# Kernel tuning notes

Hardware: AMD Instinct MI355X
Metric: run time of the kernel (lower is better)

Reference implementation:

```python
import jax, jax.numpy as jnp
import numpy as np

INPUT_DIM = 20000
UNITS = 4096
NNZ = 2_000_000
BATCH = 2048


def setup_inputs() -> dict:
    key = jax.random.key(0)
    k1, k2, k3, k4 = jax.random.split(key, 4)
    x = jax.random.normal(k1, (BATCH, INPUT_DIM), dtype=jnp.float32)
    kernel_vector = jax.random.normal(k2, (NNZ,), dtype=jnp.float32) * 0.05
    bias = jnp.zeros((UNITS,), dtype=jnp.float32)
    rows = jax.random.randint(k3, (NNZ,), 0, INPUT_DIM, dtype=jnp.int32)
    cols = jax.random.randint(k4, (NNZ,), 0, UNITS, dtype=jnp.int32)
    nonzero_ind = jnp.stack([rows, cols], axis=1)  # (NNZ, 2)
    return {"x": x, "kernel_vector": kernel_vector, "bias": bias, "nonzero_ind": nonzero_ind}


def reference(x, kernel_vector, bias, nonzero_ind):
    # scatter_nd: build dense (input_dim, units) kernel from COO representation.
    # Duplicate indices accumulate (tf.scatter_nd semantics) -> use .add.
    trans = jnp.zeros((INPUT_DIM, UNITS), dtype=kernel_vector.dtype)
    trans = trans.at[nonzero_ind[:, 0], nonzero_ind[:, 1]].add(kernel_vector)
    out = x @ trans + bias  # (batch, units)
    return jnp.tanh(out)
```

## Files before the change

kernel.cpp:

```cpp
#include <hip/hip_runtime.h>
#include <cstdint>
#include <cstddef>

#define M_DIM 2048
#define N_DIM 4096
#define K_DIM 20000
#define KP    20480
#define KZ    10240
#define NITER 80
#define WBT_BYTES  167772160UL
#define XB_OFFSET  167772160UL
#define CP_OFFSET  251658240UL

typedef __attribute__((ext_vector_type(8))) short short8;
typedef __attribute__((ext_vector_type(4))) float float4v;
typedef __attribute__((ext_vector_type(8))) unsigned short ushort8;

__device__ __forceinline__ unsigned short f2bf_rne(float f) {
    union { float f; unsigned int u; } v; v.f = f;
    unsigned int u = v.u;
    u += 0x7FFFu + ((u >> 16) & 1u);
    return (unsigned short)(u >> 16);
}

__device__ __forceinline__ float bf2f(unsigned short h) {
    union { unsigned int u; float f; } v;
    v.u = ((unsigned int)h) << 16;
    return v.f;
}

__device__ __forceinline__ void gload_lds16(const void* g, void* l) {
    __builtin_amdgcn_global_load_lds(
        (const __attribute__((address_space(1))) void*)g,
        (__attribute__((address_space(3))) void*)l, 16, 0, 0);
}

__global__ void scatter_bf16_kernel(const float* __restrict__ kv,
                                    const int* __restrict__ ind,
                                    unsigned int* __restrict__ W, int nnz) {
    int t = blockIdx.x * blockDim.x + threadIdx.x;
    if (t >= nnz) return;
    int r = ind[2 * t];
    int c = ind[2 * t + 1];
    float v = kv[t];
    size_t elem = (size_t)c * KP + r;
    unsigned int* word = &W[elem >> 1];
    const bool hi = (elem & 1) != 0;
    unsigned int old = __atomic_load_n(word, __ATOMIC_RELAXED);
    unsigned int assumed;
    do {
        assumed = old;
        unsigned short h = hi ? (unsigned short)(assumed >> 16)
                              : (unsigned short)(assumed & 0xFFFFu);
        unsigned short nh = f2bf_rne(bf2f(h) + v);
        unsigned int nw = hi ? ((assumed & 0x0000FFFFu) | ((unsigned int)nh << 16))
                             : ((assumed & 0xFFFF0000u) | (unsigned int)nh);
        old = atomicCAS(word, assumed, nw);
    } while (old != assumed);
}

__global__ void convert_kernel(const float* __restrict__ src,
                               unsigned short* __restrict__ dst) {
    size_t t = (size_t)blockIdx.x * 256 + threadIdx.x;
    int row = (int)(t / 2560);
    int c8  = (int)(t % 2560);
    ushort8 o;
    if (c8 < 2500) {
        const float4* sv = (const float4*)(src + (size_t)row * K_DIM + (size_t)c8 * 8);
        float4 a = sv[0];
        float4 b = sv[1];
        o[0] = f2bf_rne(a.x); o[1] = f2bf_rne(a.y);
        o[2] = f2bf_rne(a.z); o[3] = f2bf_rne(a.w);
        o[4] = f2bf_rne(b.x); o[5] = f2bf_rne(b.y);
        o[6] = f2bf_rne(b.z); o[7] = f2bf_rne(b.w);
    } else {
        o = (ushort8)0;
    }
    *(ushort8*)(dst + (size_t)row * KP + (size_t)c8 * 8) = o;
}

__global__ __launch_bounds__(512, 2) void gemm256_kernel(
    const unsigned short* __restrict__ A,
    const unsigned short* __restrict__ Bt,
    float* __restrict__ Cp) {

    __shared__ unsigned short L[65536];

    const int t    = threadIdx.x;
    const int w    = t >> 6;
    const int l    = t & 63;
    const int quad = l >> 4;
    const int r16  = l & 15;
    const int wm   = w >> 2;
    const int wn   = w & 3;

    const int m0 = blockIdx.y * 256;
    const int n0 = blockIdx.x * 256;
    const size_t k0 = (size_t)blockIdx.z * KZ;

    const int l4 = l >> 2;
    const int c4 = l & 3;
    const unsigned short* pA0 = A  + (size_t)(m0 + w * 32 + l4) * KP + k0 + c4 * 8;
    const unsigned short* pA1 = pA0 + (size_t)16 * KP;
    const unsigned short* pB0 = Bt + (size_t)(n0 + w * 32 + l4) * KP + k0 + c4 * 8;
    const unsigned short* pB1 = pB0 + (size_t)16 * KP;

    char* Lb = (char*)L;
    const int wdst = w << 11;

#define STAGE_A(REG) do { \
    gload_lds16(pA0, Lb + (REG) + wdst); \
    gload_lds16(pA1, Lb + (REG) + wdst + 1024); \
    pA0 += 32; pA1 += 32; } while (0)
#define STAGE_B(REG) do { \
    gload_lds16(pB0, Lb + (REG) + wdst); \
    gload_lds16(pB1, Lb + (REG) + wdst + 1024); \
    pB0 += 32; pB1 += 32; } while (0)

    const int aoff = (wm * 128 + r16) * 64 + quad * 16;
    const int boff = 32768 + (wn * 64 + r16) * 64 + quad * 16;

    float4v acc[8][4];
#pragma unroll
    for (int i = 0; i < 8; ++i)
#pragma unroll
        for (int j = 0; j < 4; ++j)
            acc[i][j] = (float4v){0.f, 0.f, 0.f, 0.f};

    short8 bfr[4], af[4];

#define VM8 asm volatile("s_waitcnt vmcnt(8)" ::: "memory")
#define VMNONE ((void)0)

#define PHASE(BASEOFF, MH, LOADB, STG, VM) do { \
    const char* base_ = Lb + (BASEOFF); \
    if (LOADB) { \
        _Pragma("unroll") \
        for (int j = 0; j < 4; ++j) \
            bfr[j] = *(const short8*)(base_ + boff + j * 1024); \
    } \
    _Pragma("unroll") \
    for (int i = 0; i < 4; ++i) \
        af[i] = *(const short8*)(base_ + aoff + (MH) * 4096 + i * 1024); \
    STG; \
    __builtin_amdgcn_s_barrier(); \
    asm volatile("s_waitcnt lgkmcnt(0)" ::: "memory"); \
    __builtin_amdgcn_s_setprio(1); \
    _Pragma("unroll") \
    for (int i = 0; i < 4; ++i) \
        _Pragma("unroll") \
        for (int j = 0; j < 4; ++j) \
            acc[(MH) * 4 + i][j] = __builtin_amdgcn_mfma_f32_16x16x32_bf16( \
                af[i], bfr[j], acc[(MH) * 4 + i][j], 0, 0, 0); \
    __builtin_amdgcn_s_setprio(0); \
    VM; \
    __builtin_amdgcn_s_barrier(); \
} while (0)

    STAGE_A(0);     STAGE_B(32768);
    STAGE_A(16384); STAGE_B(49152);
    STAGE_A(65536); STAGE_B(98304);
    asm volatile("s_waitcnt vmcnt(8)" ::: "memory");
    __builtin_amdgcn_s_barrier();

#pragma unroll 1
    for (int it = 0; it < NITER; ++it) {
        PHASE(0,     0, true,  STAGE_A(81920),  VMNONE);
        PHASE(0,     1, false, STAGE_B(114688), VM8);
        PHASE(16384, 0, true,  STAGE_A(0),      VMNONE);
        PHASE(16384, 1, false, STAGE_B(32768),  VM8);
        PHASE(65536, 0, true,  STAGE_A(16384),  VMNONE);
        PHASE(65536, 1, false, STAGE_B(49152),  VM8);
        PHASE(81920, 0, true,  STAGE_A(65536),  VMNONE);
        PHASE(81920, 1, false, STAGE_B(98304),  VM8);
    }
    asm volatile("s_waitcnt vmcnt(0)" ::: "memory");

    float* Cz = Cp + (size_t)blockIdx.z * ((size_t)M_DIM * N_DIM);
#pragma unroll
    for (int i = 0; i < 8; ++i) {
        const int row = m0 + wm * 128 + i * 16 + quad * 4;
#pragma unroll
        for (int j = 0; j < 4; ++j) {
            const int col = n0 + wn * 64 + j * 16 + r16;
#pragma unroll
            for (int r = 0; r < 4; ++r)
                Cz[(size_t)(row + r) * N_DIM + col] = acc[i][j][r];
        }
    }
#undef PHASE
#undef STAGE_A
#undef STAGE_B
#undef VM8
#undef VMNONE
}

__global__ void combine_kernel(const float* __restrict__ Cp,
                               const float* __restrict__ bias,
                               float* __restrict__ out) {
    size_t t = (size_t)blockIdx.x * 256 + threadIdx.x;
    const size_t stride = (size_t)M_DIM * N_DIM / 4;
    float4 a = ((const float4*)Cp)[t];
    float4 b = ((const float4*)Cp)[t + stride];
    float4 bv = ((const float4*)bias)[t & (N_DIM / 4 - 1)];
    float4 o;
    o.x = tanhf(a.x + b.x + bv.x);
    o.y = tanhf(a.y + b.y + bv.y);
    o.z = tanhf(a.z + b.z + bv.z);
    o.w = tanhf(a.w + b.w + bv.w);
    ((float4*)out)[t] = o;
}

extern "C" void kernel_launch(void* const* d_in, const int* in_sizes, int n_in,
                              void* d_out, int out_size, void* d_ws, size_t ws_size,
                              hipStream_t stream) {
    const float* x    = (const float*)d_in[0];
    const float* kv   = (const float*)d_in[1];
    const float* bias = (const float*)d_in[2];
    const int*   ind  = (const int*)d_in[3];
    const int nnz = in_sizes[1];

    unsigned short* Wbt = (unsigned short*)d_ws;
    unsigned short* xb  = (unsigned short*)((char*)d_ws + XB_OFFSET);
    float* Cp = (float*)((char*)d_ws + CP_OFFSET);

    hipMemsetAsync(Wbt, 0, WBT_BYTES, stream);
    scatter_bf16_kernel<<<(nnz + 255) / 256, 256, 0, stream>>>(
        kv, ind, (unsigned int*)Wbt, nnz);
    convert_kernel<<<(M_DIM * (KP / 8)) / 256, 256, 0, stream>>>(x, xb);
    gemm256_kernel<<<dim3(N_DIM / 256, M_DIM / 256, 2), 512, 0, stream>>>(
        xb, Wbt, Cp);
    combine_kernel<<<(M_DIM * N_DIM) / (256 * 4), 256, 0, stream>>>(
        Cp, bias, (float*)d_out);
}
```

Before: 662.9 us.

## Fuse weight zeroing into convert kernel and remap LDS staging layout for conflict-free reads

Replaces the separate hipMemsetAsync of the bf16 weight buffer with extra blocks in a combined zero+convert kernel, removing one launch and running the zeroing alongside the x conversion. The GEMM's global-to-LDS staging mapping changes so each 16-byte chunk lands where a lane's MFMA fragment read becomes a contiguous l*16 offset, which is meant to avoid LDS bank conflicts on fragment loads. The global loads become less contiguous per row (16 rows by 4 chunks per wave), which may change coalescing behaviour.

After: 738.9 us. +11.5%, slower.

```diff
diff --git a/kernel.cpp b/kernel.cpp
--- a/kernel.cpp
+++ b/kernel.cpp
@@ -11,6 +11,7 @@
 #define WBT_BYTES  167772160UL
 #define XB_OFFSET  167772160UL
 #define CP_OFFSET  251658240UL
+#define ZBLK 2048
 
 typedef __attribute__((ext_vector_type(8))) short short8;
 typedef __attribute__((ext_vector_type(4))) float float4v;
@@ -59,20 +60,30 @@
     } while (old != assumed);
 }
 
-__global__ void convert_kernel(const float* __restrict__ src,
-                               unsigned short* __restrict__ dst) {
-    size_t t = (size_t)blockIdx.x * 256 + threadIdx.x;
+__global__ void zero_convert_kernel(const float* __restrict__ src,
+                                    unsigned short* __restrict__ dst,
+                                    float4* __restrict__ wzero) {
+    int b = blockIdx.x;
+    if (b < ZBLK) {
+        size_t t = (size_t)b * 256 + threadIdx.x;
+        float4 z; z.x = 0.f; z.y = 0.f; z.z = 0.f; z.w = 0.f;
+        #pragma unroll
+        for (int i = 0; i < 20; ++i)
+            wzero[t + (size_t)i * (ZBLK * 256)] = z;
+        return;
+    }
+    size_t t = (size_t)(b - ZBLK) * 256 + threadIdx.x;
     int row = (int)(t / 2560);
     int c8  = (int)(t % 2560);
     ushort8 o;
     if (c8 < 2500) {
         const float4* sv = (const float4*)(src + (size_t)row * K_DIM + (size_t)c8 * 8);
         float4 a = sv[0];
-        float4 b = sv[1];
-        o[0] = f2bf_rne(a.x); o[1] = f2bf_rne(a.y);
-        o[2] = f2bf_rne(a.z); o[3] = f2bf_rne(a.w);
-        o[4] = f2bf_rne(b.x); o[5] = f2bf_rne(b.y);
-        o[6] = f2bf_rne(b.z); o[7] = f2bf_rne(b.w);
+        float4 b2 = sv[1];
+        o[0] = f2bf_rne(a.x);  o[1] = f2bf_rne(a.y);
+        o[2] = f2bf_rne(a.z);  o[3] = f2bf_rne(a.w);
+        o[4] = f2bf_rne(b2.x); o[5] = f2bf_rne(b2.y);
+        o[6] = f2bf_rne(b2.z); o[7] = f2bf_rne(b2.w);
     } else {
         o = (ushort8)0;
     }
@@ -98,11 +109,11 @@
     const int n0 = blockIdx.x * 256;
     const size_t k0 = (size_t)blockIdx.z * KZ;
 
-    const int l4 = l >> 2;
-    const int c4 = l & 3;
-    const unsigned short* pA0 = A  + (size_t)(m0 + w * 32 + l4) * KP + k0 + c4 * 8;
+    const int lr = l & 15;
+    const int lc = l >> 4;
+    const unsigned short* pA0 = A  + (size_t)(m0 + w * 32 + lr) * KP + k0 + lc * 8;
     const unsigned short* pA1 = pA0 + (size_t)16 * KP;
-    const unsigned short* pB0 = Bt + (size_t)(n0 + w * 32 + l4) * KP + k0 + c4 * 8;
+    const unsigned short* pB0 = Bt + (size_t)(n0 + w * 32 + lr) * KP + k0 + lc * 8;
     const unsigned short* pB1 = pB0 + (size_t)16 * KP;
 
     char* Lb = (char*)L;
@@ -117,8 +128,8 @@
     gload_lds16(pB1, Lb + (REG) + wdst + 1024); \
     pB0 += 32; pB1 += 32; } while (0)
 
-    const int aoff = (wm * 128 + r16) * 64 + quad * 16;
-    const int boff = 32768 + (wn * 64 + r16) * 64 + quad * 16;
+    const int aoff = wm * 8192 + l * 16;
+    const int boff = 32768 + wn * 4096 + l * 16;
 
     float4v acc[8][4];
 #pragma unroll
@@ -224,10 +235,10 @@
     unsigned short* xb  = (unsigned short*)((char*)d_ws + XB_OFFSET);
     float* Cp = (float*)((char*)d_ws + CP_OFFSET);
 
-    hipMemsetAsync(Wbt, 0, WBT_BYTES, stream);
+    zero_convert_kernel<<<ZBLK + (M_DIM * (KP / 8)) / 256, 256, 0, stream>>>(
+        x, xb, (float4*)Wbt);
     scatter_bf16_kernel<<<(nnz + 255) / 256, 256, 0, stream>>>(
         kv, ind, (unsigned int*)Wbt, nnz);
-    convert_kernel<<<(M_DIM * (KP / 8)) / 256, 256, 0, stream>>>(x, xb);
     gemm256_kernel<<<dim3(N_DIM / 256, M_DIM / 256, 2), 512, 0, stream>>>(
         xb, Wbt, Cp);
     combine_kernel<<<(M_DIM * N_DIM) / (256 * 4), 256, 0, stream>>>(
```

## Switch GEMM LDS tiles to 64-wide K with XOR swizzle and double buffering

Applied to the files above, without the earlier changes.

Restructures the GEMM main loop so each LDS stage holds a 256x64 K-slab of A and B, laid out with an XOR swizzle on 16-byte chunks to avoid bank conflicts on the MFMA fragment reads. The four-stage, 32-wide pipeline becomes a two-buffer scheme. Global-to-LDS copies are spread across the four phases of each tile, and the wait thresholds change to match. Wider K tiles mean fewer barriers per unit of K work, but the shallower double buffering may expose more memory latency.

Result: faster. 640.9 us (-3.3%).

```diff
diff --git a/kernel.cpp b/kernel.cpp
--- a/kernel.cpp
+++ b/kernel.cpp
@@ -7,7 +7,7 @@
 #define K_DIM 20000
 #define KP    20480
 #define KZ    10240
-#define NITER 80
+#define NTILE 160
 #define WBT_BYTES  167772160UL
 #define XB_OFFSET  167772160UL
 #define CP_OFFSET  251658240UL
@@ -98,27 +98,31 @@
     const int n0 = blockIdx.x * 256;
     const size_t k0 = (size_t)blockIdx.z * KZ;
 
-    const int l4 = l >> 2;
-    const int c4 = l & 3;
-    const unsigned short* pA0 = A  + (size_t)(m0 + w * 32 + l4) * KP + k0 + c4 * 8;
-    const unsigned short* pA1 = pA0 + (size_t)16 * KP;
-    const unsigned short* pB0 = Bt + (size_t)(n0 + w * 32 + l4) * KP + k0 + c4 * 8;
-    const unsigned short* pB1 = pB0 + (size_t)16 * KP;
+    const int lr8 = l >> 3;
+    const int sl  = (l & 7) ^ lr8;
+    const int w1024 = w << 10;
+
+    const unsigned short* pA0 = A  + (size_t)(m0 +   0 + w * 8 + lr8) * KP + k0 + sl * 8;
+    const unsigned short* pA1 = A  + (size_t)(m0 +  64 + w * 8 + lr8) * KP + k0 + sl * 8;
+    const unsigned short* pA2 = A  + (size_t)(m0 + 128 + w * 8 + lr8) * KP + k0 + sl * 8;
+    const unsigned short* pA3 = A  + (size_t)(m0 + 192 + w * 8 + lr8) * KP + k0 + sl * 8;
+    const unsigned short* pB0 = Bt + (size_t)(n0 +   0 + w * 8 + lr8) * KP + k0 + sl * 8;
+    const unsigned short* pB1 = Bt + (size_t)(n0 +  64 + w * 8 + lr8) * KP + k0 + sl * 8;
+    const unsigned short* pB2 = Bt + (size_t)(n0 + 128 + w * 8 + lr8) * KP + k0 + sl * 8;
+    const unsigned short* pB3 = Bt + (size_t)(n0 + 192 + w * 8 + lr8) * KP + k0 + sl * 8;
 
     char* Lb = (char*)L;
-    const int wdst = w << 11;
-
-#define STAGE_A(REG) do { \
-    gload_lds16(pA0, Lb + (REG) + wdst); \
-    gload_lds16(pA1, Lb + (REG) + wdst + 1024); \
-    pA0 += 32; pA1 += 32; } while (0)
-#define STAGE_B(REG) do { \
-    gload_lds16(pB0, Lb + (REG) + wdst); \
-    gload_lds16(pB1, Lb + (REG) + wdst + 1024); \
-    pB0 += 32; pB1 += 32; } while (0)
-
-    const int aoff = (wm * 128 + r16) * 64 + quad * 16;
-    const int boff = 32768 + (wn * 64 + r16) * 64 + quad * 16;
+
+#define STG_A(OB, Q, P) do { \
+    gload_lds16(P, Lb + (OB) + (Q) * 8192 + w1024); P += 64; } while (0)
+#define STG_B(OB, Q, P) do { \
+    gload_lds16(P, Lb + (OB) + 32768 + (Q) * 8192 + w1024); P += 64; } while (0)
+
+    const int h   = r16 & 7;
+    const int so0 = ((quad ^ h) << 4);
+    const int so1 = (((4 | quad) ^ h) << 4);
+    const int aoff = wm * 16384 + r16 * 128;
+    const int boff = 32768 + wn * 8192 + r16 * 128;
 
     float4v acc[8][4];
 #pragma unroll
@@ -129,19 +133,19 @@
 
     short8 bfr[4], af[4];
 
-#define VM8 asm volatile("s_waitcnt vmcnt(8)" ::: "memory")
+#define VM2 asm volatile("s_waitcnt vmcnt(2)" ::: "memory")
 #define VMNONE ((void)0)
 
-#define PHASE(BASEOFF, MH, LOADB, STG, VM) do { \
-    const char* base_ = Lb + (BASEOFF); \
+#define PHASE(BUF, MH, SO, LOADB, STG, VM) do { \
+    const char* base_ = Lb + (BUF); \
     if (LOADB) { \
         _Pragma("unroll") \
         for (int j = 0; j < 4; ++j) \
-            bfr[j] = *(const short8*)(base_ + boff + j * 1024); \
+            bfr[j] = *(const short8*)(base_ + boff + j * 2048 + (SO)); \
     } \
     _Pragma("unroll") \
     for (int i = 0; i < 4; ++i) \
-        af[i] = *(const short8*)(base_ + aoff + (MH) * 4096 + i * 1024); \
+        af[i] = *(const short8*)(base_ + aoff + (MH) * 8192 + i * 2048 + (SO)); \
     STG; \
     __builtin_amdgcn_s_barrier(); \
     asm volatile("s_waitcnt lgkmcnt(0)" ::: "memory"); \
@@ -157,22 +161,23 @@
     __builtin_amdgcn_s_barrier(); \
 } while (0)
 
-    STAGE_A(0);     STAGE_B(32768);
-    STAGE_A(16384); STAGE_B(49152);
-    STAGE_A(65536); STAGE_B(98304);
-    asm volatile("s_waitcnt vmcnt(8)" ::: "memory");
+#define TILE(BUF, OB) do { \
+    PHASE(BUF, 0, so0, true,  { STG_A(OB, 0, pA0); STG_A(OB, 1, pA1); }, VMNONE); \
+    PHASE(BUF, 1, so0, false, { STG_A(OB, 2, pA2); STG_A(OB, 3, pA3); }, VMNONE); \
+    PHASE(BUF, 0, so1, true,  { STG_B(OB, 2, pB2); STG_B(OB, 3, pB3); }, VMNONE); \
+    PHASE(BUF, 1, so1, false, { STG_B(BUF, 0, pB0); STG_B(BUF, 1, pB1); }, VM2); \
+} while (0)
+
+    STG_A(0, 0, pA0); STG_A(0, 1, pA1); STG_A(0, 2, pA2); STG_A(0, 3, pA3);
+    STG_B(0, 0, pB0); STG_B(0, 1, pB1); STG_B(0, 2, pB2); STG_B(0, 3, pB3);
+    STG_B(65536, 0, pB0); STG_B(65536, 1, pB1);
+    asm volatile("s_waitcnt vmcnt(2)" ::: "memory");
     __builtin_amdgcn_s_barrier();
 
 #pragma unroll 1
-    for (int it = 0; it < NITER; ++it) {
-        PHASE(0,     0, true,  STAGE_A(81920),  VMNONE);
-        PHASE(0,     1, false, STAGE_B(114688), VM8);
-        PHASE(16384, 0, true,  STAGE_A(0),      VMNONE);
-        PHASE(16384, 1, false, STAGE_B(32768),  VM8);
-        PHASE(65536, 0, true,  STAGE_A(16384),  VMNONE);
-        PHASE(65536, 1, false, STAGE_B(49152),  VM8);
-        PHASE(81920, 0, true,  STAGE_A(65536),  VMNONE);
-        PHASE(81920, 1, false, STAGE_B(98304),  VM8);
+    for (int it = 0; it < NTILE / 2; ++it) {
+        TILE(0, 65536);
+        TILE(65536, 0);
     }
     asm volatile("s_waitcnt vmcnt(0)" ::: "memory");
 
@@ -188,10 +193,11 @@
                 Cz[(size_t)(row + r) * N_DIM + col] = acc[i][j][r];
         }
     }
+#undef TILE
 #undef PHASE
-#undef STAGE_A
-#undef STAGE_B
-#undef VM8
+#undef STG_A
+#undef STG_B
+#undef VM2
 #undef VMNONE
 }
 
```
